# Optimization experiments

Measured on AMD Instinct MI355X. Metric: run time of the kernel, lower is better.

## Reference

```python
import jax, jax.numpy as jnp
import numpy as np

B, S, D, H, BLEN, FF = 4, 4096, 1024, 16, 256, 4096
DH = D // H
NEG = -1e9
EPS = 1e-6


def setup_inputs() -> dict:
    key = jax.random.key(0)
    ks = jax.random.split(key, 8)
    s = 0.02
    return {
        "X": jax.random.normal(ks[0], (B, S, D), jnp.float32),
        "Wq": jax.random.normal(ks[1], (D, D), jnp.float32) * s,
        "Wk": jax.random.normal(ks[2], (D, D), jnp.float32) * s,
        "Wv": jax.random.normal(ks[3], (D, D), jnp.float32) * s,
        "Wo": jax.random.normal(ks[4], (D, D), jnp.float32) * s,
        "g_attn": jnp.ones((D,), jnp.float32),
        "b_attn": jnp.zeros((D,), jnp.float32),
        "W1": jax.random.normal(ks[5], (D, FF), jnp.float32) * s,
        "b1": jnp.zeros((FF,), jnp.float32),
        "W2": jax.random.normal(ks[6], (FF, D), jnp.float32) * s,
        "b2": jnp.zeros((D,), jnp.float32),
        "g_ffn": jnp.ones((D,), jnp.float32),
        "b_ffn": jnp.zeros((D,), jnp.float32),
    }


def _layernorm(x, g, b):
    mu = jnp.mean(x, axis=-1, keepdims=True)
    var = jnp.mean(jnp.square(x - mu), axis=-1, keepdims=True)
    return (x - mu) * jax.lax.rsqrt(var + EPS) * g + b


def _local_attn(X, Wq, Wk, Wv, Wo):
    def split_heads(y):  # [B,S,D] -> [B,H,S,DH]
        return y.reshape(B, S, H, DH).transpose(0, 2, 1, 3)

    q = split_heads(X @ Wq) * (DH ** -0.5)
    k = split_heads(X @ Wk)
    v = split_heads(X @ Wv)

    nb = S // BLEN  # S is a multiple of BLEN, so the torch pad is a no-op
    q = q.reshape(B, H, nb, BLEN, DH)
    k = k.reshape(B, H, nb, BLEN, DH)
    v = v.reshape(B, H, nb, BLEN, DH)

    # First block: plain causal attention within block 0.
    causal = NEG * jnp.triu(jnp.ones((BLEN, BLEN), jnp.float32), 1)
    logits0 = jnp.einsum('bhkd,bhqd->bhqk', k[:, :, 0], q[:, :, 0]) + causal
    out0 = jax.nn.softmax(logits0, axis=-1) @ v[:, :, 0]  # [B,H,BLEN,DH]

    # Tail blocks attend to [previous block, current block].
    local_k = jnp.concatenate([k[:, :, :-1], k[:, :, 1:]], axis=3)  # [B,H,nb-1,2B,DH]
    local_v = jnp.concatenate([v[:, :, :-1], v[:, :, 1:]], axis=3)
    tail_q = q[:, :, 1:]
    bias = NEG * jnp.triu(jnp.ones((BLEN, 2 * BLEN), jnp.float32), BLEN + 1)
    logits = jnp.einsum('bhnkd,bhnqd->bhnqk', local_k, tail_q) + bias
    tail = jnp.einsum('bhnqk,bhnkd->bhnqd', jax.nn.softmax(logits, axis=-1), local_v)
    tail = tail.reshape(B, H, S - BLEN, DH)

    res = jnp.concatenate([out0, tail], axis=2)       # [B,H,S,DH]
    res = res.transpose(0, 2, 1, 3).reshape(B, S, D)  # merge heads
    return res @ Wo


def reference(X, Wq, Wk, Wv, Wo, g_attn, b_attn, W1, b1, W2, b2, g_ffn, b_ffn):
    y = _local_attn(X, Wq, Wk, Wv, Wo)
    X = _layernorm(y + X, g_attn, b_attn)
    y = jax.nn.relu(X @ W1 + b1) @ W2 + b2
    X = _layernorm(y + X, g_ffn, b_ffn)
    return X
```

## Files before the change

kernel.cpp:

```cpp
#include <hip/hip_runtime.h>
#include <stdint.h>

#define B_    4
#define S_    4096
#define D_    1024
#define H_    16
#define DH_   64
#define BLEN_ 256
#define FF_   4096
#define M_    16384

typedef unsigned short u16;
typedef __attribute__((ext_vector_type(8))) short s8v;
typedef __attribute__((ext_vector_type(4))) short s4v;
typedef __attribute__((ext_vector_type(4))) float f4v;

#define MFMA32(A,B,C) __builtin_amdgcn_mfma_f32_16x16x32_bf16(A,B,C,0,0,0)
#define BAR() asm volatile("s_barrier" ::: "memory")
#define SCHEDB() __builtin_amdgcn_sched_barrier(0)

__device__ __forceinline__ f4v mfma16(s4v a, s4v b, f4v c) {
#if defined(__HIP_DEVICE_COMPILE__)
#if __has_builtin(__builtin_amdgcn_mfma_f32_16x16x16bf16_1k)
  return __builtin_amdgcn_mfma_f32_16x16x16bf16_1k(a, b, c, 0, 0, 0);
#elif __has_builtin(__builtin_amdgcn_mfma_f32_16x16x16_bf16_1k)
  return __builtin_amdgcn_mfma_f32_16x16x16_bf16_1k(a, b, c, 0, 0, 0);
#elif __has_builtin(__builtin_amdgcn_mfma_f32_16x16x16_bf16)
  return __builtin_amdgcn_mfma_f32_16x16x16_bf16(a, b, c, 0, 0, 0);
#else
  f4v d;
  asm volatile("v_mfma_f32_16x16x16_bf16 %0, %1, %2, %3"
               : "=v"(d) : "v"(a), "v"(b), "v"(c));
  return d;
#endif
#else
  (void)a; (void)b; return c;
#endif
}

__device__ __forceinline__ u16 f2b(float f) {
  union { float f; unsigned u; } v; v.f = f;
  unsigned r = v.u + 0x7fffu + ((v.u >> 16) & 1u);
  return (u16)(r >> 16);
}
__device__ __forceinline__ float b2f(u16 h) {
  union { unsigned u; float f; } v; v.u = ((unsigned)h) << 16; return v.f;
}

__device__ __forceinline__ void gld16(const void* gp, void* lp) {
  __builtin_amdgcn_global_load_lds(
      (const __attribute__((address_space(1))) void*)(uintptr_t)gp,
      (__attribute__((address_space(3))) void*)(uintptr_t)lp, 16, 0, 0);
}


__global__ __launch_bounds__(256) void k_castx(const float* __restrict__ in, u16* __restrict__ out) {
  long i = (long)blockIdx.x * 256 + threadIdx.x;
  float4 v = ((const float4*)in)[i];
  s4v o; o[0] = (short)f2b(v.x); o[1] = (short)f2b(v.y);
  o[2] = (short)f2b(v.z); o[3] = (short)f2b(v.w);
  *(s4v*)(out + i * 4) = o;
}

__global__ __launch_bounds__(256) void k_wt(const float* __restrict__ in, u16* __restrict__ out,
                                            int K, int N, float scale) {
  long i = (long)blockIdx.x * 256 + threadIdx.x;
  if (i >= (long)K * N) return;
  int k = (int)(i / N), n = (int)(i % N);
  out[(long)n * K + k] = f2b(in[i] * scale);
}

template<int EPI>
__global__ __launch_bounds__(512, 2) void k_gemm256(
    const u16* __restrict__ A, const u16* __restrict__ Bt,
    const float* __restrict__ bias, const void* __restrict__ res,
    u16* __restrict__ out, int N, int K) {
  __shared__ __align__(16) u16 sA[2][16384];
  __shared__ __align__(16) u16 sB[2][16384];
  const int t = threadIdx.x, lane = t & 63, w = t >> 6;
  const int wm = w >> 2, wn = w & 3;
  const int nwg = gridDim.x, cpx = nwg >> 3, orig = blockIdx.x;
  const int wg = (orig & 7) * cpx + (orig >> 3);
  const int mb = wg & 63, nb = wg >> 6;
  const int m0 = mb << 8, n0 = nb << 8;
  const int NT = K >> 6;

  const int srow = lane >> 3;
  const int scol = ((lane & 7) ^ srow) << 3;
  const u16* gA = A + (size_t)(m0 + srow) * K + scol;
  const u16* gB = Bt + (size_t)(n0 + srow) * K + scol;

  auto stA = [&](int d, int h, int kt) {
#pragma unroll
    for (int i = 0; i < 2; i++) {
      int c = i * 8 + w;
      gld16(gA + (size_t)(h * 128 + c * 8) * K + kt * 64, &sA[d][h * 8192 + c * 512]);
    }
  };
  auto stB = [&](int d, int h, int kt) {
#pragma unroll
    for (int i = 0; i < 2; i++) {
      int c = i * 8 + w;
      gld16(gB + (size_t)(h * 128 + c * 8) * K + kt * 64, &sB[d][h * 8192 + c * 512]);
    }
  };

  const int swz = (lane & 7) << 4;
  const int g8b = (lane >> 4) << 4;
  const int r16 = lane & 15;
  auto rdA = [&](int d, int mt, int kh) -> s8v {
    int byt = (mt * 32 + wm * 16 + r16) * 128 + ((kh * 64 + g8b) ^ swz);
    return *(const s8v*)((const char*)sA[d] + byt);
  };
  auto rdB = [&](int d, int nt, int kh) -> s8v {
    int byt = (nt * 64 + wn * 16 + r16) * 128 + ((kh * 64 + g8b) ^ swz);
    return *(const s8v*)((const char*)sB[d] + byt);
  };

  f4v acc[8][4];
  f4v zz = {0.f, 0.f, 0.f, 0.f};
#pragma unroll
  for (int i = 0; i < 8; i++)
#pragma unroll
    for (int j = 0; j < 4; j++) acc[i][j] = zz;

  stA(0, 0, 0); stB(0, 0, 0);
  stB(0, 1, 0); stA(0, 1, 0);
  stA(1, 0, 1); stB(1, 0, 1);
  asm volatile("s_waitcnt vmcnt(4)" ::: "memory");
  BAR();

  for (int j = 0; j < NT; ++j) {
    const int d = j & 1, nd = d ^ 1;
    const bool s1 = (j + 1 < NT), s2 = (j + 2 < NT);
    s8v af[4][2], b0[2][2], b1[2][2];

#pragma unroll
    for (int mt = 0; mt < 4; mt++) { af[mt][0] = rdA(d, mt, 0); af[mt][1] = rdA(d, mt, 1); }
#pragma unroll
    for (int nt = 0; nt < 2; nt++) { b0[nt][0] = rdB(d, nt, 0); b0[nt][1] = rdB(d, nt, 1); }
    if (s1) stB(nd, 1, j + 1);
    BAR();
    __builtin_amdgcn_s_setprio(1);
#pragma unroll
    for (int mt = 0; mt < 4; mt++)
#pragma unroll
      for (int nt = 0; nt < 2; nt++) {
        acc[mt][nt] = MFMA32(af[mt][0], b0[nt][0], acc[mt][nt]);
        acc[mt][nt] = MFMA32(af[mt][1], b0[nt][1], acc[mt][nt]);
      }
    __builtin_amdgcn_s_setprio(0);
    SCHEDB();
    BAR();

#pragma unroll
    for (int nt = 0; nt < 2; nt++) { b1[nt][0] = rdB(d, nt + 2, 0); b1[nt][1] = rdB(d, nt + 2, 1); }
    if (s1) stA(nd, 1, j + 1);
    BAR();
    __builtin_amdgcn_s_setprio(1);
#pragma unroll
    for (int mt = 0; mt < 4; mt++)
#pragma unroll
      for (int nt = 0; nt < 2; nt++) {
        acc[mt][nt + 2] = MFMA32(af[mt][0], b1[nt][0], acc[mt][nt + 2]);
        acc[mt][nt + 2] = MFMA32(af[mt][1], b1[nt][1], acc[mt][nt + 2]);
      }
    __builtin_amdgcn_s_setprio(0);
    SCHEDB();
    BAR();

#pragma unroll
    for (int mt = 0; mt < 4; mt++) { af[mt][0] = rdA(d, mt + 4, 0); af[mt][1] = rdA(d, mt + 4, 1); }
    if (s2) stA(d, 0, j + 2);
    BAR();
    __builtin_amdgcn_s_setprio(1);
#pragma unroll
    for (int mt = 0; mt < 4; mt++)
#pragma unroll
      for (int nt = 0; nt < 2; nt++) {
        acc[mt + 4][nt] = MFMA32(af[mt][0], b0[nt][0], acc[mt + 4][nt]);
        acc[mt + 4][nt] = MFMA32(af[mt][1], b0[nt][1], acc[mt + 4][nt]);
      }
    __builtin_amdgcn_s_setprio(0);
    SCHEDB();
    BAR();

    if (s2) stB(d, 0, j + 2);
    BAR();
    __builtin_amdgcn_s_setprio(1);
#pragma unroll
    for (int mt = 0; mt < 4; mt++)
#pragma unroll
      for (int nt = 0; nt < 2; nt++) {
        acc[mt + 4][nt + 2] = MFMA32(af[mt][0], b1[nt][0], acc[mt + 4][nt + 2]);
        acc[mt + 4][nt + 2] = MFMA32(af[mt][1], b1[nt][1], acc[mt + 4][nt + 2]);
      }
    __builtin_amdgcn_s_setprio(0);
    SCHEDB();
    if (s2) asm volatile("s_waitcnt vmcnt(4)" ::: "memory");
    else    asm volatile("s_waitcnt vmcnt(0)" ::: "memory");
    BAR();
  }

  const int g4 = (lane >> 4) << 2;
#pragma unroll
  for (int mt = 0; mt < 8; mt++) {
#pragma unroll
    for (int nt = 0; nt < 4; nt++) {
      const int col = n0 + nt * 64 + wn * 16 + r16;
      const long rbase = m0 + mt * 32 + wm * 16 + g4;
      float bcol = 0.f;
      if constexpr (EPI == 2 || EPI == 3) bcol = bias[col];
#pragma unroll
      for (int r = 0; r < 4; r++) {
        long idx = (rbase + r) * (long)N + col;
        float v = acc[mt][nt][r];
        if constexpr (EPI == 1) v += ((const float*)res)[idx];
        if constexpr (EPI == 2) { v += bcol; v = fmaxf(v, 0.f); }
        if constexpr (EPI == 3) { v += bcol + b2f(((const u16*)res)[idx]); }
        out[idx] = f2b(v);
      }
    }
  }
}

__global__ __launch_bounds__(256) void k_attn(const u16* __restrict__ QKV, u16* __restrict__ Aout) {
  __shared__ __align__(16) u16 sK[64 * 64];
  __shared__ __align__(16) u16 sVT[64 * 64];
  const int t = threadIdx.x, lane = t & 63, w = t >> 6;
  const int qblock = blockIdx.x;
  const int b = blockIdx.y >> 4, h = blockIdx.y & 15;
  const int qcol = lane & 15, g = lane >> 4, g4 = g << 2;
  const int win = (qblock == 0) ? 0 : (qblock - 1) * BLEN_;
  const int nch = (qblock == 0) ? 4 : 8;
  const int qbw = qblock * BLEN_ + w * 64;
  const long rowbase = (long)b * S_;
  const int LDQ = 3072;

  s8v qf[4][2];
#pragma unroll
  for (int nt = 0; nt < 4; nt++)
#pragma unroll
    for (int kh = 0; kh < 2; kh++)
      qf[nt][kh] = *(const s8v*)(QKV + (rowbase + qbw + nt * 16 + qcol) * LDQ + h * DH_ + kh * 32 + (g << 3));

  f4v zz = {0.f, 0.f, 0.f, 0.f};
  f4v acc[4][4];
#pragma unroll
  for (int i = 0; i < 4; i++)
#pragma unroll
    for (int j = 0; j < 4; j++) acc[i][j] = zz;
  float mrow[4] = {-1e30f, -1e30f, -1e30f, -1e30f};
  float lrow[4] = {0.f, 0.f, 0.f, 0.f};

  for (int c = 0; c < nch; ++c) {
    const int kb = win + c * 64;
    __syncthreads();
#pragma unroll
    for (int p = 0; p < 2; p++) {
      int key = p * 32 + (t >> 3);
      int d8 = (t & 7) << 3;
      s8v kv = *(const s8v*)(QKV + (rowbase + kb + key) * LDQ + 1024 + h * DH_ + d8);
      int bo = key * 128 + d8 * 2; bo ^= (key & 7) << 4;
      *(s8v*)((char*)sK + bo) = kv;
    }
#pragma unroll
    for (int p = 0; p < 2; p++) {
      int key = (t & 31) + (p << 5);
      int d8 = (t >> 5) << 3;
      s8v vv = *(const s8v*)(QKV + (rowbase + kb + key) * LDQ + 2048 + h * DH_ + d8);
#pragma unroll
      for (int j = 0; j < 8; j++) {
        int dh = d8 + j;
        int bo = dh * 128 + key * 2; bo ^= (dh & 7) << 3;
        *(u16*)((char*)sVT + bo) = (u16)vv[j];
      }
    }
    __syncthreads();
    if (kb > qbw + 63) continue;

    f4v st[4][4];
#pragma unroll
    for (int i = 0; i < 4; i++)
#pragma unroll
      for (int j = 0; j < 4; j++) st[i][j] = zz;
#pragma unroll
    for (int kh = 0; kh < 2; kh++) {
#pragma unroll
      for (int mt = 0; mt < 4; mt++) {
        int key = mt * 16 + qcol;
        int bo = key * 128 + kh * 64 + (g << 4); bo ^= (key & 7) << 4;
        s8v kf = *(const s8v*)((const char*)sK + bo);
#pragma unroll
        for (int nt = 0; nt < 4; nt++) st[mt][nt] = MFMA32(kf, qf[nt][kh], st[mt][nt]);
      }
    }
    if (kb + 63 > qbw) {
#pragma unroll
      for (int mt = 0; mt < 4; mt++) {
        int kbase = kb + mt * 16 + g4;
#pragma unroll
        for (int nt = 0; nt < 4; nt++) {
          int qabs = qbw + nt * 16 + qcol;
#pragma unroll
          for (int r = 0; r < 4; r++)
            if (kbase + r > qabs) st[mt][nt][r] = -1e30f;
        }
      }
    }
    s4v pf[4][4];
#pragma unroll
    for (int nt = 0; nt < 4; nt++) {
      float cm = -1e30f;
#pragma unroll
      for (int mt = 0; mt < 4; mt++)
#pragma unroll
        for (int r = 0; r < 4; r++) cm = fmaxf(cm, st[mt][nt][r]);
      cm = fmaxf(cm, __shfl_xor(cm, 16));
      cm = fmaxf(cm, __shfl_xor(cm, 32));
      float mnew = fmaxf(mrow[nt], cm);
      float sc = __expf(mrow[nt] - mnew);
      mrow[nt] = mnew;
      float ps = 0.f;
#pragma unroll
      for (int kt = 0; kt < 4; kt++) {
        s4v pp;
#pragma unroll
        for (int r = 0; r < 4; r++) {
          float sv = st[kt][nt][r];
          float p = (sv > -1e29f) ? __expf(sv - mnew) : 0.f;
          ps += p;
          pp[r] = (short)f2b(p);
        }
        pf[nt][kt] = pp;
      }
      ps += __shfl_xor(ps, 16);
      ps += __shfl_xor(ps, 32);
      lrow[nt] = lrow[nt] * sc + ps;
#pragma unroll
      for (int dt = 0; dt < 4; dt++) acc[dt][nt] *= sc;
    }
#pragma unroll
    for (int dt = 0; dt < 4; dt++) {
      int dh = dt * 16 + qcol;
#pragma unroll
      for (int kt = 0; kt < 4; kt++) {
        int bo = dh * 128 + kt * 32 + (g << 3); bo ^= (dh & 7) << 3;
        s4v vf = *(const s4v*)((const char*)sVT + bo);
#pragma unroll
        for (int nt = 0; nt < 4; nt++) acc[dt][nt] = mfma16(vf, pf[nt][kt], acc[dt][nt]);
      }
    }
  }

#pragma unroll
  for (int nt = 0; nt < 4; nt++) {
    float inv = 1.f / lrow[nt];
    long qrow = rowbase + qbw + nt * 16 + qcol;
#pragma unroll
    for (int dt = 0; dt < 4; dt++) {
      s4v o;
#pragma unroll
      for (int r = 0; r < 4; r++) o[r] = (short)f2b(acc[dt][nt][r] * inv);
      *(s4v*)(Aout + qrow * D_ + h * DH_ + dt * 16 + g4) = o;
    }
  }
}

template<int OUTB>
__global__ __launch_bounds__(256) void k_ln(const u16* __restrict__ in, const float* __restrict__ gw,
                                            const float* __restrict__ bw, float* __restrict__ outf,
                                            u16* __restrict__ outb) {
  const int t = threadIdx.x, lane = t & 63, w = t >> 6;
  const long base = (long)blockIdx.x * D_;
  s4v xv = *(const s4v*)(in + base + t * 4);
  float v0 = b2f((u16)xv[0]), v1 = b2f((u16)xv[1]), v2 = b2f((u16)xv[2]), v3 = b2f((u16)xv[3]);
  float s = v0 + v1 + v2 + v3;
  float s2 = v0 * v0 + v1 * v1 + v2 * v2 + v3 * v3;
#pragma unroll
  for (int off = 1; off < 64; off <<= 1) { s += __shfl_xor(s, off); s2 += __shfl_xor(s2, off); }
  __shared__ float red[8];
  if (lane == 0) { red[w] = s; red[4 + w] = s2; }
  __syncthreads();
  s = red[0] + red[1] + red[2] + red[3];
  s2 = red[4] + red[5] + red[6] + red[7];
  float mu = s * (1.f / D_);
  float var = s2 * (1.f / D_) - mu * mu;
  float rstd = rsqrtf(var + 1e-6f);
  float4 gv = ((const float4*)gw)[t];
  float4 bv = ((const float4*)bw)[t];
  float o0 = (v0 - mu) * rstd * gv.x + bv.x;
  float o1 = (v1 - mu) * rstd * gv.y + bv.y;
  float o2 = (v2 - mu) * rstd * gv.z + bv.z;
  float o3 = (v3 - mu) * rstd * gv.w + bv.w;
  if constexpr (OUTB) {
    s4v o; o[0] = (short)f2b(o0); o[1] = (short)f2b(o1); o[2] = (short)f2b(o2); o[3] = (short)f2b(o3);
    *(s4v*)(outb + base + t * 4) = o;
  } else {
    float4 o; o.x = o0; o.y = o1; o.z = o2; o.w = o3;
    *(float4*)(outf + base + t * 4) = o;
  }
}


extern "C" void kernel_launch(void* const* d_in, const int* in_sizes, int n_in,
                              void* d_out, int out_size, void* d_ws, size_t ws_size,
                              hipStream_t stream) {
  const float* X      = (const float*)d_in[0];
  const float* Wq     = (const float*)d_in[1];
  const float* Wk     = (const float*)d_in[2];
  const float* Wv     = (const float*)d_in[3];
  const float* Wo     = (const float*)d_in[4];
  const float* g_attn = (const float*)d_in[5];
  const float* b_attn = (const float*)d_in[6];
  const float* W1     = (const float*)d_in[7];
  const float* b1     = (const float*)d_in[8];
  const float* W2     = (const float*)d_in[9];
  const float* b2     = (const float*)d_in[10];
  const float* g_ffn  = (const float*)d_in[11];
  const float* b_ffn  = (const float*)d_in[12];
  float* out = (float*)d_out;

  char* ws = (char*)d_ws;
  const size_t MB = 1ull << 20;
  u16* WqkvT = (u16*)(ws + 0 * MB);
  u16* WoT   = (u16*)(ws + 6 * MB);
  u16* W1T   = (u16*)(ws + 8 * MB);
  u16* W2T   = (u16*)(ws + 16 * MB);
  u16* Xb    = (u16*)(ws + 24 * MB);
  u16* QKVb  = (u16*)(ws + 56 * MB);
  u16* Ab    = (u16*)(ws + 152 * MB);
  u16* Yb    = (u16*)(ws + 184 * MB);
  u16* Mid   = QKVb;

  dim3 b256(256), b512(512);
  k_wt<<<dim3(4096),  b256, 0, stream>>>(Wq, WqkvT,                1024, 1024, 0.125f);
  k_wt<<<dim3(4096),  b256, 0, stream>>>(Wk, WqkvT + 1024 * 1024,  1024, 1024, 1.0f);
  k_wt<<<dim3(4096),  b256, 0, stream>>>(Wv, WqkvT + 2048 * 1024,  1024, 1024, 1.0f);
  k_wt<<<dim3(4096),  b256, 0, stream>>>(Wo, WoT, 1024, 1024, 1.0f);
  k_wt<<<dim3(16384), b256, 0, stream>>>(W1, W1T, 1024, 4096, 1.0f);
  k_wt<<<dim3(16384), b256, 0, stream>>>(W2, W2T, 4096, 1024, 1.0f);
  k_castx<<<dim3(16384), b256, 0, stream>>>(X, Xb);

  k_gemm256<0><<<dim3(768), b512, 0, stream>>>(Xb, WqkvT, nullptr, nullptr, QKVb, 3072, 1024);
  k_attn<<<dim3(16, B_ * H_), b256, 0, stream>>>(QKVb, Ab);
  k_gemm256<1><<<dim3(256), b512, 0, stream>>>(Ab, WoT, nullptr, X, Yb, 1024, 1024);
  k_ln<1><<<dim3(16384), b256, 0, stream>>>(Yb, g_attn, b_attn, nullptr, Xb);
  k_gemm256<2><<<dim3(1024), b512, 0, stream>>>(Xb, W1T, b1, nullptr, Mid, 4096, 1024);
  k_gemm256<3><<<dim3(256), b512, 0, stream>>>(Mid, W2T, b2, Xb, Yb, 1024, 4096);
  k_ln<0><<<dim3(16384), b256, 0, stream>>>(Yb, g_ffn, b_ffn, out, nullptr);

  (void)in_sizes; (void)n_in; (void)out_size; (void)ws_size;
}
```

Baseline: 673.3 us.

## Restructure GEMM main loop to prefetch LDS fragments and drop barriers

Reworks the 256x256 GEMM inner loop so the shared-memory fragment reads for the next phase happen before the current MFMA block. The first A/B fragments of the next k-tile are loaded at the end of each iteration. Intermediate barriers and sched_barriers are removed, and K becomes a template parameter so the trip count is compile-time. This is meant to hide LDS latency behind MFMA work and cut synchronisation. In exchange it needs more registers (an extra A fragment set), and the reduced barriers could race with the global-to-LDS stores.

```diff
diff --git a/kernel.cpp b/kernel.cpp
--- a/kernel.cpp
+++ b/kernel.cpp
@@ -17,7 +17,6 @@
 
 #define MFMA32(A,B,C) __builtin_amdgcn_mfma_f32_16x16x32_bf16(A,B,C,0,0,0)
 #define BAR() asm volatile("s_barrier" ::: "memory")
-#define SCHEDB() __builtin_amdgcn_sched_barrier(0)
 
 __device__ __forceinline__ f4v mfma16(s4v a, s4v b, f4v c) {
 #if defined(__HIP_DEVICE_COMPILE__)
@@ -70,11 +69,11 @@
   out[(long)n * K + k] = f2b(in[i] * scale);
 }
 
-template<int EPI>
+template<int EPI, int K>
 __global__ __launch_bounds__(512, 2) void k_gemm256(
     const u16* __restrict__ A, const u16* __restrict__ Bt,
     const float* __restrict__ bias, const void* __restrict__ res,
-    u16* __restrict__ out, int N, int K) {
+    u16* __restrict__ out, int N) {
   __shared__ __align__(16) u16 sA[2][16384];
   __shared__ __align__(16) u16 sB[2][16384];
   const int t = threadIdx.x, lane = t & 63, w = t >> 6;
@@ -83,7 +82,7 @@
   const int wg = (orig & 7) * cpx + (orig >> 3);
   const int mb = wg & 63, nb = wg >> 6;
   const int m0 = mb << 8, n0 = nb << 8;
-  const int NT = K >> 6;
+  constexpr int NT = K >> 6;
 
   const int srow = lane >> 3;
   const int scol = ((lane & 7) ^ srow) << 3;
@@ -124,23 +123,24 @@
 #pragma unroll
     for (int j = 0; j < 4; j++) acc[i][j] = zz;
 
-  stA(0, 0, 0); stB(0, 0, 0);
-  stB(0, 1, 0); stA(0, 1, 0);
+  stA(0, 0, 0); stB(0, 0, 0); stA(0, 1, 0); stB(0, 1, 0);
   stA(1, 0, 1); stB(1, 0, 1);
   asm volatile("s_waitcnt vmcnt(4)" ::: "memory");
   BAR();
 
+  s8v af[4][2], af2[4][2], b0[2][2], b1[2][2];
+#pragma unroll
+  for (int mt = 0; mt < 4; mt++) { af[mt][0] = rdA(0, mt, 0); af[mt][1] = rdA(0, mt, 1); }
+#pragma unroll
+  for (int nt = 0; nt < 2; nt++) { b0[nt][0] = rdB(0, nt, 0); b0[nt][1] = rdB(0, nt, 1); }
+
   for (int j = 0; j < NT; ++j) {
     const int d = j & 1, nd = d ^ 1;
     const bool s1 = (j + 1 < NT), s2 = (j + 2 < NT);
-    s8v af[4][2], b0[2][2], b1[2][2];
-
-#pragma unroll
-    for (int mt = 0; mt < 4; mt++) { af[mt][0] = rdA(d, mt, 0); af[mt][1] = rdA(d, mt, 1); }
-#pragma unroll
-    for (int nt = 0; nt < 2; nt++) { b0[nt][0] = rdB(d, nt, 0); b0[nt][1] = rdB(d, nt, 1); }
+
+#pragma unroll
+    for (int nt = 0; nt < 2; nt++) { b1[nt][0] = rdB(d, nt + 2, 0); b1[nt][1] = rdB(d, nt + 2, 1); }
     if (s1) stB(nd, 1, j + 1);
-    BAR();
     __builtin_amdgcn_s_setprio(1);
 #pragma unroll
     for (int mt = 0; mt < 4; mt++)
@@ -150,13 +150,10 @@
         acc[mt][nt] = MFMA32(af[mt][1], b0[nt][1], acc[mt][nt]);
       }
     __builtin_amdgcn_s_setprio(0);
-    SCHEDB();
-    BAR();
-
-#pragma unroll
-    for (int nt = 0; nt < 2; nt++) { b1[nt][0] = rdB(d, nt + 2, 0); b1[nt][1] = rdB(d, nt + 2, 1); }
+
+#pragma unroll
+    for (int mt = 0; mt < 4; mt++) { af2[mt][0] = rdA(d, mt + 4, 0); af2[mt][1] = rdA(d, mt + 4, 1); }
     if (s1) stA(nd, 1, j + 1);
-    BAR();
     __builtin_amdgcn_s_setprio(1);
 #pragma unroll
     for (int mt = 0; mt < 4; mt++)
@@ -166,40 +163,39 @@
         acc[mt][nt + 2] = MFMA32(af[mt][1], b1[nt][1], acc[mt][nt + 2]);
       }
     __builtin_amdgcn_s_setprio(0);
-    SCHEDB();
     BAR();
 
-#pragma unroll
-    for (int mt = 0; mt < 4; mt++) { af[mt][0] = rdA(d, mt + 4, 0); af[mt][1] = rdA(d, mt + 4, 1); }
     if (s2) stA(d, 0, j + 2);
+    __builtin_amdgcn_s_setprio(1);
+#pragma unroll
+    for (int mt = 0; mt < 4; mt++)
+#pragma unroll
+      for (int nt = 0; nt < 2; nt++) {
+        acc[mt + 4][nt] = MFMA32(af2[mt][0], b0[nt][0], acc[mt + 4][nt]);
+        acc[mt + 4][nt] = MFMA32(af2[mt][1], b0[nt][1], acc[mt + 4][nt]);
+      }
+    __builtin_amdgcn_s_setprio(0);
     BAR();
+
+    if (s2) stB(d, 0, j + 2);
     __builtin_amdgcn_s_setprio(1);
 #pragma unroll
     for (int mt = 0; mt < 4; mt++)
 #pragma unroll
       for (int nt = 0; nt < 2; nt++) {
-        acc[mt + 4][nt] = MFMA32(af[mt][0], b0[nt][0], acc[mt + 4][nt]);
-        acc[mt + 4][nt] = MFMA32(af[mt][1], b0[nt][1], acc[mt + 4][nt]);
+        acc[mt + 4][nt + 2] = MFMA32(af2[mt][0], b1[nt][0], acc[mt + 4][nt + 2]);
+        acc[mt + 4][nt + 2] = MFMA32(af2[mt][1], b1[nt][1], acc[mt + 4][nt + 2]);
       }
     __builtin_amdgcn_s_setprio(0);
-    SCHEDB();
-    BAR();
-
-    if (s2) stB(d, 0, j + 2);
-    BAR();
-    __builtin_amdgcn_s_setprio(1);
-#pragma unroll
-    for (int mt = 0; mt < 4; mt++)
-#pragma unroll
-      for (int nt = 0; nt < 2; nt++) {
-        acc[mt + 4][nt + 2] = MFMA32(af[mt][0], b1[nt][0], acc[mt + 4][nt + 2]);
-        acc[mt + 4][nt + 2] = MFMA32(af[mt][1], b1[nt][1], acc[mt + 4][nt + 2]);
-      }
-    __builtin_amdgcn_s_setprio(0);
-    SCHEDB();
     if (s2) asm volatile("s_waitcnt vmcnt(4)" ::: "memory");
     else    asm volatile("s_waitcnt vmcnt(0)" ::: "memory");
     BAR();
+    if (s1) {
+#pragma unroll
+      for (int mt = 0; mt < 4; mt++) { af[mt][0] = rdA(nd, mt, 0); af[mt][1] = rdA(nd, mt, 1); }
+#pragma unroll
+      for (int nt = 0; nt < 2; nt++) { b0[nt][0] = rdB(nd, nt, 0); b0[nt][1] = rdB(nd, nt, 1); }
+    }
   }
 
   const int g4 = (lane >> 4) << 2;
@@ -442,12 +438,12 @@
   k_wt<<<dim3(16384), b256, 0, stream>>>(W2, W2T, 4096, 1024, 1.0f);
   k_castx<<<dim3(16384), b256, 0, stream>>>(X, Xb);
 
-  k_gemm256<0><<<dim3(768), b512, 0, stream>>>(Xb, WqkvT, nullptr, nullptr, QKVb, 3072, 1024);
+  k_gemm256<0, 1024><<<dim3(768), b512, 0, stream>>>(Xb, WqkvT, nullptr, nullptr, QKVb, 3072);
   k_attn<<<dim3(16, B_ * H_), b256, 0, stream>>>(QKVb, Ab);
-  k_gemm256<1><<<dim3(256), b512, 0, stream>>>(Ab, WoT, nullptr, X, Yb, 1024, 1024);
+  k_gemm256<1, 1024><<<dim3(256), b512, 0, stream>>>(Ab, WoT, nullptr, X, Yb, 1024);
   k_ln<1><<<dim3(16384), b256, 0, stream>>>(Yb, g_attn, b_attn, nullptr, Xb);
-  k_gemm256<2><<<dim3(1024), b512, 0, stream>>>(Xb, W1T, b1, nullptr, Mid, 4096, 1024);
-  k_gemm256<3><<<dim3(256), b512, 0, stream>>>(Mid, W2T, b2, Xb, Yb, 1024, 4096);
+  k_gemm256<2, 1024><<<dim3(1024), b512, 0, stream>>>(Xb, W1T, b1, nullptr, Mid, 4096);
+  k_gemm256<3, 4096><<<dim3(256), b512, 0, stream>>>(Mid, W2T, b2, Xb, Yb, 1024);
   k_ln<0><<<dim3(16384), b256, 0, stream>>>(Yb, g_ffn, b_ffn, out, nullptr);
 
   (void)in_sizes; (void)n_in; (void)out_size; (void)ws_size;
```

Measured after the change: 661.5 us. About the same (-1.8%).
